# Kernel optimization log

Measured on AMD Instinct MI355X. Metric: run time of the kernel, lower is better.

## Reference

```python
import jax, jax.numpy as jnp
import numpy as np

TARGET_LEN = 288
HIDDEN = 128
INPUT_SIZE = 7
OUT_SIZE = 3  # len(quantiles)
BATCH = 1024
SEQ = 288


def _lstm_cell(x_t, h, c, Wih, Whh, b):
    # PyTorch LSTM gate order: i, f, g, o; z: (B, 4H)
    z = x_t @ Wih.T + h @ Whh.T + b
    i, f, g, o = jnp.split(z, 4, axis=-1)
    c_new = jax.nn.sigmoid(f) * c + jax.nn.sigmoid(i) * jnp.tanh(g)
    h_new = jax.nn.sigmoid(o) * jnp.tanh(c_new)
    return h_new, c_new


def setup_inputs() -> dict:
    key = jax.random.key(0)
    ks = jax.random.split(key, 11)
    s = 0.08  # ~ 1/sqrt(hidden), matches torch LSTM uniform init scale
    return {
        "x": jax.random.normal(ks[0], (BATCH, SEQ, INPUT_SIZE), jnp.float32),
        "enc_Wih": jax.random.normal(ks[1], (4 * HIDDEN, INPUT_SIZE), jnp.float32) * s,
        "enc_Whh": jax.random.normal(ks[2], (4 * HIDDEN, HIDDEN), jnp.float32) * s,
        "enc_bih": jax.random.normal(ks[3], (4 * HIDDEN,), jnp.float32) * s,
        "enc_bhh": jax.random.normal(ks[4], (4 * HIDDEN,), jnp.float32) * s,
        "dec_Wih": jax.random.normal(ks[5], (4 * HIDDEN, OUT_SIZE), jnp.float32) * s,
        "dec_Whh": jax.random.normal(ks[6], (4 * HIDDEN, HIDDEN), jnp.float32) * s,
        "dec_bih": jax.random.normal(ks[7], (4 * HIDDEN,), jnp.float32) * s,
        "dec_bhh": jax.random.normal(ks[8], (4 * HIDDEN,), jnp.float32) * s,
        "out_W": jax.random.normal(ks[9], (OUT_SIZE, HIDDEN), jnp.float32) * s,
        "out_b": jax.random.normal(ks[10], (OUT_SIZE,), jnp.float32) * s,
    }


def reference(x, enc_Wih, enc_Whh, enc_bih, enc_bhh,
              dec_Wih, dec_Whh, dec_bih, dec_bhh, out_W, out_b):
    B = x.shape[0]
    H = enc_Whh.shape[1]
    b_enc = enc_bih + enc_bhh
    b_dec = dec_bih + dec_bhh

    # ----- encoder LSTM over the input sequence -----
    def enc_step(carry, x_t):
        h, c = carry
        h, c = _lstm_cell(x_t, h, c, enc_Wih, enc_Whh, b_enc)
        return (h, c), None

    h0 = jnp.zeros((B, H), x.dtype)
    (h_enc, c_enc), _ = jax.lax.scan(enc_step, (h0, h0), jnp.swapaxes(x, 0, 1))

    # returned state, so every step restarts from (h_enc, c_enc); only the
    # previous output (quantiles) feeds back. Dropout is identity (eval). -----
    def dec_step(y_prev, _):
        h, _c = _lstm_cell(y_prev, h_enc, c_enc, dec_Wih, dec_Whh, b_dec)
        y = h @ out_W.T + out_b  # (B, OUT_SIZE)
        return y, y

    y0 = jnp.zeros((B, out_W.shape[0]), x.dtype)
    _, ys = jax.lax.scan(dec_step, y0, None, length=TARGET_LEN)  # (T, B, O)
    return jnp.swapaxes(ys, 0, 1)  # (B, TARGET_LEN, OUT_SIZE)
```

## Files before the change

### kernel.cpp

```cpp
#include <hip/hip_runtime.h>

#define SEQ 288
#define INP 7
#define HID 128
#define TLEN 288
#define OUTD 3
#define XW (SEQ * INP)

typedef _Float16 f16x8 __attribute__((ext_vector_type(8)));
typedef float f32x4 __attribute__((ext_vector_type(4)));

__device__ __forceinline__ float fast_sigmoid(float x) {
    float e = __expf(-x);
    return __builtin_amdgcn_rcpf(1.0f + e);
}
__device__ __forceinline__ float fast_tanh(float x) {
    float e = __expf(-2.0f * x);
    return 2.0f * __builtin_amdgcn_rcpf(1.0f + e) - 1.0f;
}

template<int CTRL, int RM>
__device__ __forceinline__ float dpp_add(float v) {
    int t = __builtin_amdgcn_update_dpp(0, __float_as_int(v), CTRL, RM, 0xF, true);
    return v + __int_as_float(t);
}
__device__ __forceinline__ float wave_sum(float v) {
    v = dpp_add<0xB1, 0xF>(v);
    v = dpp_add<0x4E, 0xF>(v);
    v = dpp_add<0x124, 0xF>(v);
    v = dpp_add<0x128, 0xF>(v);
    v = dpp_add<0x142, 0xA>(v);
    v = dpp_add<0x143, 0xC>(v);
    return __int_as_float(__builtin_amdgcn_readlane(__float_as_int(v), 63));
}

__device__ __forceinline__ float redist4(f32x4 s) {
    int r0 = __float_as_int(s[0]), r1 = __float_as_int(s[1]);
    int r2 = __float_as_int(s[2]), r3 = __float_as_int(s[3]);
    auto p02 = __builtin_amdgcn_permlane32_swap(r0, r2, false, false);
    auto p13 = __builtin_amdgcn_permlane32_swap(r1, r3, false, false);
#if __has_builtin(__builtin_amdgcn_permlane16_swap)
    auto q = __builtin_amdgcn_permlane16_swap(p02[0], p13[0], false, false);
    return __int_as_float(q[0]);
#else
    float n0 = __int_as_float(p02[0]);
    float n1 = __int_as_float(p13[0]);
    int lane = threadIdx.x & 63;
    float tshf = __shfl(n1, lane ^ 16);
    return (lane & 16) ? tshf : n0;
#endif
}

__global__ __launch_bounds__(512, 2)
void enc_dec_kernel(const float* __restrict__ x,
                    const float* __restrict__ eWih, const float* __restrict__ eWhh,
                    const float* __restrict__ ebih, const float* __restrict__ ebhh,
                    const float* __restrict__ dWih, const float* __restrict__ dWhh,
                    const float* __restrict__ dbih, const float* __restrict__ dbhh,
                    const float* __restrict__ oW,  const float* __restrict__ ob,
                    float* __restrict__ out)
{
    __shared__ __align__(16) _Float16 hbuf[2][4][16][40];
    __shared__ __align__(16) _Float16 xf16[SEQ + 1][4][8];
    __shared__ float zbl[4][4][HID];
    __shared__ float cl[4][HID];

    const int tid  = threadIdx.x;
    const int wave = tid >> 6;
    const int lane = tid & 63;
    const int col  = lane & 15;
    const int grp  = lane >> 4;
    const int u    = wave * 16 + col;
    const int bb   = grp;
    const int b0   = blockIdx.x * 4;

    {
        _Float16* hb = &hbuf[0][0][0][0];
        for (int i = tid; i < 2 * 4 * 16 * 40; i += 512) hb[i] = (_Float16)0.f;
        _Float16* xp = &xf16[SEQ][0][0];
        if (tid < 32) xp[tid] = (_Float16)0.f;
    }
    for (int i = tid; i < 4 * XW; i += 512) {
        int b = i / XW, r = i % XW;
        int t = r / INP, j = r % INP;
        xf16[t][b][j] = (_Float16)x[(size_t)(b0 + b) * XW + r];
    }
    for (int i = tid; i < SEQ * 4; i += 512)
        xf16[i >> 2][i & 3][7] = (_Float16)1.0f;

    f16x8 wfrag[4][5];
    #pragma unroll
    for (int gt = 0; gt < 4; ++gt) {
        const int row = gt * HID + u;
        #pragma unroll
        for (int kc = 0; kc < 4; ++kc) {
            const float* wr = eWhh + (size_t)row * HID + kc * 32 + grp * 8;
            f16x8 wf;
            #pragma unroll
            for (int e = 0; e < 8; ++e) wf[e] = (_Float16)wr[e];
            wfrag[gt][kc] = wf;
        }
        {
            f16x8 wf;
            #pragma unroll
            for (int e = 0; e < 8; ++e) {
                int j = grp * 8 + e;
                float v = 0.f;
                if (j < INP)       v = eWih[(size_t)row * INP + j];
                else if (j == 7)   v = ebih[row] + ebhh[row];
                wf[e] = (_Float16)v;
            }
            wfrag[gt][4] = wf;
        }
    }

    __syncthreads();

    float cc = 0.f;
    const f32x4 zero = (f32x4){0.f, 0.f, 0.f, 0.f};

    f32x4 accX[4];
    {
        f16x8 ax0 = *(const f16x8*)&xf16[0][col & 3][0];
        #pragma unroll
        for (int gt = 0; gt < 4; ++gt)
            accX[gt] = __builtin_amdgcn_mfma_f32_16x16x32_f16(ax0, wfrag[gt][4], zero, 0, 0, 0);
    }

    #define ENC_STEP(T, CUR, NXT)                                                     \
    {                                                                                 \
        f16x8 af0 = *(const f16x8*)&hbuf[CUR][0][col][grp * 8];                       \
        f16x8 af1 = *(const f16x8*)&hbuf[CUR][1][col][grp * 8];                       \
        f16x8 af2 = *(const f16x8*)&hbuf[CUR][2][col][grp * 8];                       \
        f16x8 af3 = *(const f16x8*)&hbuf[CUR][3][col][grp * 8];                       \
        f32x4 acc[4];                                                                 \
        _Pragma("unroll")                                                             \
        for (int gt = 0; gt < 4; ++gt) {                                              \
            acc[gt] = __builtin_amdgcn_mfma_f32_16x16x32_f16(af0, wfrag[gt][0], accX[gt], 0, 0, 0); \
            acc[gt] = __builtin_amdgcn_mfma_f32_16x16x32_f16(af1, wfrag[gt][1], acc[gt], 0, 0, 0);  \
            acc[gt] = __builtin_amdgcn_mfma_f32_16x16x32_f16(af2, wfrag[gt][2], acc[gt], 0, 0, 0);  \
            acc[gt] = __builtin_amdgcn_mfma_f32_16x16x32_f16(af3, wfrag[gt][3], acc[gt], 0, 0, 0);  \
        }                                                                             \
        f16x8 axn = *(const f16x8*)&xf16[(T) + 1][col & 3][0];                        \
        _Pragma("unroll")                                                             \
        for (int gt = 0; gt < 4; ++gt)                                                \
            accX[gt] = __builtin_amdgcn_mfma_f32_16x16x32_f16(axn, wfrag[gt][4], zero, 0, 0, 0);    \
        float zi = redist4(acc[0]);                                                   \
        float zf = redist4(acc[1]);                                                   \
        float zg = redist4(acc[2]);                                                   \
        float zo = redist4(acc[3]);                                                   \
        float si = fast_sigmoid(zi);                                                  \
        float sf = fast_sigmoid(zf);                                                  \
        float tg = fast_tanh(zg);                                                     \
        float so = fast_sigmoid(zo);                                                  \
        cc = sf * cc + si * tg;                                                       \
        float h = so * fast_tanh(cc);                                                 \
        hbuf[NXT][u >> 5][bb][u & 31] = (_Float16)h;                                  \
        __syncthreads();                                                              \
    }

    for (int t = 0; t < SEQ; t += 2) {
        ENC_STEP(t, 0, 1)
        ENC_STEP(t + 1, 1, 0)
    }
    #undef ENC_STEP

    #pragma unroll
    for (int gt = 0; gt < 4; ++gt) {
        const int row = gt * HID + u;
        #pragma unroll
        for (int kc = 0; kc < 4; ++kc) {
            const float* wr = dWhh + (size_t)row * HID + kc * 32 + grp * 8;
            f16x8 wf;
            #pragma unroll
            for (int e = 0; e < 8; ++e) wf[e] = (_Float16)wr[e];
            wfrag[gt][kc] = wf;
        }
    }
    {
        f16x8 af0 = *(const f16x8*)&hbuf[0][0][col][grp * 8];
        f16x8 af1 = *(const f16x8*)&hbuf[0][1][col][grp * 8];
        f16x8 af2 = *(const f16x8*)&hbuf[0][2][col][grp * 8];
        f16x8 af3 = *(const f16x8*)&hbuf[0][3][col][grp * 8];
        #pragma unroll
        for (int gt = 0; gt < 4; ++gt) {
            float bd = dbih[gt * HID + u] + dbhh[gt * HID + u];
            f32x4 acc = (f32x4){bd, bd, bd, bd};
            acc = __builtin_amdgcn_mfma_f32_16x16x32_f16(af0, wfrag[gt][0], acc, 0, 0, 0);
            acc = __builtin_amdgcn_mfma_f32_16x16x32_f16(af1, wfrag[gt][1], acc, 0, 0, 0);
            acc = __builtin_amdgcn_mfma_f32_16x16x32_f16(af2, wfrag[gt][2], acc, 0, 0, 0);
            acc = __builtin_amdgcn_mfma_f32_16x16x32_f16(af3, wfrag[gt][3], acc, 0, 0, 0);
            zbl[gt][bb][u] = redist4(acc);
        }
        cl[bb][u] = cc;
    }
    __syncthreads();

    if (wave >= 4) return;
    {
        const int b = wave;
        const int u0 = lane, u1 = 64 + lane;
        float zb0[4], zb1[4], wd0[4][3], wd1[4][3];
        #pragma unroll
        for (int gt = 0; gt < 4; ++gt) {
            zb0[gt] = zbl[gt][b][u0];
            zb1[gt] = zbl[gt][b][u1];
            #pragma unroll
            for (int j = 0; j < 3; ++j) {
                wd0[gt][j] = dWih[(size_t)(gt * HID + u0) * 3 + j];
                wd1[gt][j] = dWih[(size_t)(gt * HID + u1) * 3 + j];
            }
        }
        const float c0 = cl[b][u0], c1 = cl[b][u1];
        float ow0[3], ow1[3];
        #pragma unroll
        for (int j = 0; j < 3; ++j) {
            ow0[j] = oW[j * HID + u0];
            ow1[j] = oW[j * HID + u1];
        }
        const float ob0 = ob[0], ob1 = ob[1], ob2 = ob[2];

        float y0 = 0.f, y1 = 0.f, y2 = 0.f;
        float* orow = out + (size_t)(b0 + b) * (TLEN * OUTD);

        for (int t = 0; t < TLEN; ++t) {
            float z0[4], z1[4];
            #pragma unroll
            for (int gt = 0; gt < 4; ++gt) {
                z0[gt] = zb0[gt] + wd0[gt][0] * y0 + wd0[gt][1] * y1 + wd0[gt][2] * y2;
                z1[gt] = zb1[gt] + wd1[gt][0] * y0 + wd1[gt][1] * y1 + wd1[gt][2] * y2;
            }
            float si0 = fast_sigmoid(z0[0]), sf0 = fast_sigmoid(z0[1]);
            float tg0 = fast_tanh(z0[2]),    so0 = fast_sigmoid(z0[3]);
            float si1 = fast_sigmoid(z1[0]), sf1 = fast_sigmoid(z1[1]);
            float tg1 = fast_tanh(z1[2]),    so1 = fast_sigmoid(z1[3]);
            float cd0 = sf0 * c0 + si0 * tg0;
            float cd1 = sf1 * c1 + si1 * tg1;
            float hd0 = so0 * fast_tanh(cd0);
            float hd1 = so1 * fast_tanh(cd1);
            float p0 = ow0[0] * hd0 + ow1[0] * hd1;
            float p1 = ow0[1] * hd0 + ow1[1] * hd1;
            float p2 = ow0[2] * hd0 + ow1[2] * hd1;
            y0 = wave_sum(p0) + ob0;
            y1 = wave_sum(p1) + ob1;
            y2 = wave_sum(p2) + ob2;
            if (lane < 3)
                orow[t * OUTD + lane] = (lane == 0) ? y0 : (lane == 1) ? y1 : y2;
        }
    }
}

extern "C" void kernel_launch(void* const* d_in, const int* in_sizes, int n_in,
                              void* d_out, int out_size, void* d_ws, size_t ws_size,
                              hipStream_t stream) {
    (void)in_sizes; (void)n_in; (void)d_ws; (void)ws_size; (void)out_size;
    enc_dec_kernel<<<256, 512, 0, stream>>>(
        (const float*)d_in[0],
        (const float*)d_in[1], (const float*)d_in[2],
        (const float*)d_in[3], (const float*)d_in[4],
        (const float*)d_in[5], (const float*)d_in[6],
        (const float*)d_in[7], (const float*)d_in[8],
        (const float*)d_in[9], (const float*)d_in[10],
        (float*)d_out);
}
```

Measured before the change: 290.6 us.

## Split batch to two rows per block with four waves each owning thirty-two units

Each block now handles two batch rows instead of four, using 256 threads, and launches 512 blocks. Each wave computes two 16-unit tiles of gates and merges the MFMA outputs with an extra permlane swap. The aim is to spread the serial recurrence across more CUs and to use smaller per-step barriers. In exchange, half of every MFMA's batch rows carry padding, so useful matrix throughput per instruction is halved, and each wave holds twice as many weight fragments in registers.

```diff
diff --git a/kernel.cpp b/kernel.cpp
--- a/kernel.cpp
+++ b/kernel.cpp
@@ -6,6 +6,7 @@
 #define TLEN 288
 #define OUTD 3
 #define XW (SEQ * INP)
+#define BPB 2
 
 typedef _Float16 f16x8 __attribute__((ext_vector_type(8)));
 typedef float f32x4 __attribute__((ext_vector_type(4)));
@@ -51,7 +52,15 @@
 #endif
 }
 
-__global__ __launch_bounds__(512, 2)
+__device__ __forceinline__ float combine2(f32x4 a0, f32x4 a1) {
+    float z0 = redist4(a0);
+    float z1 = redist4(a1);
+    auto pr = __builtin_amdgcn_permlane32_swap(__float_as_int(z0),
+                                               __float_as_int(z1), false, false);
+    return __int_as_float(pr[0]);
+}
+
+__global__ __launch_bounds__(256, 2)
 void enc_dec_kernel(const float* __restrict__ x,
                     const float* __restrict__ eWih, const float* __restrict__ eWhh,
                     const float* __restrict__ ebih, const float* __restrict__ ebhh,
@@ -61,56 +70,59 @@
                     float* __restrict__ out)
 {
     __shared__ __align__(16) _Float16 hbuf[2][4][16][40];
-    __shared__ __align__(16) _Float16 xf16[SEQ + 1][4][8];
-    __shared__ float zbl[4][4][HID];
-    __shared__ float cl[4][HID];
+    __shared__ __align__(16) _Float16 xf16[SEQ + 1][BPB][8];
+    __shared__ float zbl[4][BPB][HID];
+    __shared__ float cl[BPB][HID];
 
     const int tid  = threadIdx.x;
     const int wave = tid >> 6;
     const int lane = tid & 63;
     const int col  = lane & 15;
     const int grp  = lane >> 4;
-    const int u    = wave * 16 + col;
-    const int bb   = grp;
-    const int b0   = blockIdx.x * 4;
+    const int bb   = (lane >> 4) & 1;
+    const int uu   = wave * 32 + (lane >> 5) * 16 + (lane & 15);
+    const int b0   = blockIdx.x * BPB;
 
     {
         _Float16* hb = &hbuf[0][0][0][0];
-        for (int i = tid; i < 2 * 4 * 16 * 40; i += 512) hb[i] = (_Float16)0.f;
+        for (int i = tid; i < 2 * 4 * 16 * 40; i += 256) hb[i] = (_Float16)0.f;
         _Float16* xp = &xf16[SEQ][0][0];
-        if (tid < 32) xp[tid] = (_Float16)0.f;
-    }
-    for (int i = tid; i < 4 * XW; i += 512) {
+        if (tid < BPB * 8) xp[tid] = (_Float16)0.f;
+    }
+    for (int i = tid; i < BPB * XW; i += 256) {
         int b = i / XW, r = i % XW;
         int t = r / INP, j = r % INP;
         xf16[t][b][j] = (_Float16)x[(size_t)(b0 + b) * XW + r];
     }
-    for (int i = tid; i < SEQ * 4; i += 512)
-        xf16[i >> 2][i & 3][7] = (_Float16)1.0f;
-
-    f16x8 wfrag[4][5];
+    for (int i = tid; i < SEQ * BPB; i += 256)
+        xf16[i / BPB][i % BPB][7] = (_Float16)1.0f;
+
+    f16x8 wfrag[4][2][5];
     #pragma unroll
     for (int gt = 0; gt < 4; ++gt) {
-        const int row = gt * HID + u;
-        #pragma unroll
-        for (int kc = 0; kc < 4; ++kc) {
-            const float* wr = eWhh + (size_t)row * HID + kc * 32 + grp * 8;
-            f16x8 wf;
-            #pragma unroll
-            for (int e = 0; e < 8; ++e) wf[e] = (_Float16)wr[e];
-            wfrag[gt][kc] = wf;
-        }
-        {
-            f16x8 wf;
-            #pragma unroll
-            for (int e = 0; e < 8; ++e) {
-                int j = grp * 8 + e;
-                float v = 0.f;
-                if (j < INP)       v = eWih[(size_t)row * INP + j];
-                else if (j == 7)   v = ebih[row] + ebhh[row];
-                wf[e] = (_Float16)v;
-            }
-            wfrag[gt][4] = wf;
+        #pragma unroll
+        for (int tl = 0; tl < 2; ++tl) {
+            const int row = gt * HID + wave * 32 + tl * 16 + col;
+            #pragma unroll
+            for (int kc = 0; kc < 4; ++kc) {
+                const float* wr = eWhh + (size_t)row * HID + kc * 32 + grp * 8;
+                f16x8 wf;
+                #pragma unroll
+                for (int e = 0; e < 8; ++e) wf[e] = (_Float16)wr[e];
+                wfrag[gt][tl][kc] = wf;
+            }
+            {
+                f16x8 wf;
+                #pragma unroll
+                for (int e = 0; e < 8; ++e) {
+                    int j = grp * 8 + e;
+                    float v = 0.f;
+                    if (j < INP)       v = eWih[(size_t)row * INP + j];
+                    else if (j == 7)   v = ebih[row] + ebhh[row];
+                    wf[e] = (_Float16)v;
+                }
+                wfrag[gt][tl][4] = wf;
+            }
         }
     }
 
@@ -119,12 +131,14 @@
     float cc = 0.f;
     const f32x4 zero = (f32x4){0.f, 0.f, 0.f, 0.f};
 
-    f32x4 accX[4];
-    {
-        f16x8 ax0 = *(const f16x8*)&xf16[0][col & 3][0];
+    f32x4 accX[4][2];
+    {
+        f16x8 ax0 = *(const f16x8*)&xf16[0][col & 1][0];
         #pragma unroll
         for (int gt = 0; gt < 4; ++gt)
-            accX[gt] = __builtin_amdgcn_mfma_f32_16x16x32_f16(ax0, wfrag[gt][4], zero, 0, 0, 0);
+            #pragma unroll
+            for (int tl = 0; tl < 2; ++tl)
+                accX[gt][tl] = __builtin_amdgcn_mfma_f32_16x16x32_f16(ax0, wfrag[gt][tl][4], zero, 0, 0, 0);
     }
 
     #define ENC_STEP(T, CUR, NXT)                                                     \
@@ -133,29 +147,34 @@
         f16x8 af1 = *(const f16x8*)&hbuf[CUR][1][col][grp * 8];                       \
         f16x8 af2 = *(const f16x8*)&hbuf[CUR][2][col][grp * 8];                       \
         f16x8 af3 = *(const f16x8*)&hbuf[CUR][3][col][grp * 8];                       \
-        f32x4 acc[4];                                                                 \
+        f16x8 axn = *(const f16x8*)&xf16[(T) + 1][col & 1][0];                        \
+        f32x4 acc[4][2];                                                              \
         _Pragma("unroll")                                                             \
         for (int gt = 0; gt < 4; ++gt) {                                              \
-            acc[gt] = __builtin_amdgcn_mfma_f32_16x16x32_f16(af0, wfrag[gt][0], accX[gt], 0, 0, 0); \
-            acc[gt] = __builtin_amdgcn_mfma_f32_16x16x32_f16(af1, wfrag[gt][1], acc[gt], 0, 0, 0);  \
-            acc[gt] = __builtin_amdgcn_mfma_f32_16x16x32_f16(af2, wfrag[gt][2], acc[gt], 0, 0, 0);  \
-            acc[gt] = __builtin_amdgcn_mfma_f32_16x16x32_f16(af3, wfrag[gt][3], acc[gt], 0, 0, 0);  \
+            _Pragma("unroll")                                                         \
+            for (int tl = 0; tl < 2; ++tl) {                                          \
+                acc[gt][tl] = __builtin_amdgcn_mfma_f32_16x16x32_f16(af0, wfrag[gt][tl][0], accX[gt][tl], 0, 0, 0); \
+                acc[gt][tl] = __builtin_amdgcn_mfma_f32_16x16x32_f16(af1, wfrag[gt][tl][1], acc[gt][tl], 0, 0, 0);  \
+                acc[gt][tl] = __builtin_amdgcn_mfma_f32_16x16x32_f16(af2, wfrag[gt][tl][2], acc[gt][tl], 0, 0, 0);  \
+                acc[gt][tl] = __builtin_amdgcn_mfma_f32_16x16x32_f16(af3, wfrag[gt][tl][3], acc[gt][tl], 0, 0, 0);  \
+            }                                                                         \
         }                                                                             \
-        f16x8 axn = *(const f16x8*)&xf16[(T) + 1][col & 3][0];                        \
         _Pragma("unroll")                                                             \
         for (int gt = 0; gt < 4; ++gt)                                                \
-            accX[gt] = __builtin_amdgcn_mfma_f32_16x16x32_f16(axn, wfrag[gt][4], zero, 0, 0, 0);    \
-        float zi = redist4(acc[0]);                                                   \
-        float zf = redist4(acc[1]);                                                   \
-        float zg = redist4(acc[2]);                                                   \
-        float zo = redist4(acc[3]);                                                   \
+            _Pragma("unroll")                                                         \
+            for (int tl = 0; tl < 2; ++tl)                                            \
+                accX[gt][tl] = __builtin_amdgcn_mfma_f32_16x16x32_f16(axn, wfrag[gt][tl][4], zero, 0, 0, 0); \
+        float zi = combine2(acc[0][0], acc[0][1]);                                    \
+        float zf = combine2(acc[1][0], acc[1][1]);                                    \
+        float zg = combine2(acc[2][0], acc[2][1]);                                    \
+        float zo = combine2(acc[3][0], acc[3][1]);                                    \
         float si = fast_sigmoid(zi);                                                  \
         float sf = fast_sigmoid(zf);                                                  \
         float tg = fast_tanh(zg);                                                     \
         float so = fast_sigmoid(zo);                                                  \
         cc = sf * cc + si * tg;                                                       \
         float h = so * fast_tanh(cc);                                                 \
-        hbuf[NXT][u >> 5][bb][u & 31] = (_Float16)h;                                  \
+        hbuf[NXT][uu >> 5][bb][uu & 31] = (_Float16)h;                                \
         __syncthreads();                                                              \
     }
 
@@ -167,14 +186,17 @@
 
     #pragma unroll
     for (int gt = 0; gt < 4; ++gt) {
-        const int row = gt * HID + u;
-        #pragma unroll
-        for (int kc = 0; kc < 4; ++kc) {
-            const float* wr = dWhh + (size_t)row * HID + kc * 32 + grp * 8;
-            f16x8 wf;
-            #pragma unroll
-            for (int e = 0; e < 8; ++e) wf[e] = (_Float16)wr[e];
-            wfrag[gt][kc] = wf;
+        #pragma unroll
+        for (int tl = 0; tl < 2; ++tl) {
+            const int row = gt * HID + wave * 32 + tl * 16 + col;
+            #pragma unroll
+            for (int kc = 0; kc < 4; ++kc) {
+                const float* wr = dWhh + (size_t)row * HID + kc * 32 + grp * 8;
+                f16x8 wf;
+                #pragma unroll
+                for (int e = 0; e < 8; ++e) wf[e] = (_Float16)wr[e];
+                wfrag[gt][tl][kc] = wf;
+            }
         }
     }
     {
@@ -182,21 +204,29 @@
         f16x8 af1 = *(const f16x8*)&hbuf[0][1][col][grp * 8];
         f16x8 af2 = *(const f16x8*)&hbuf[0][2][col][grp * 8];
         f16x8 af3 = *(const f16x8*)&hbuf[0][3][col][grp * 8];
+        f32x4 acc[4][2];
         #pragma unroll
         for (int gt = 0; gt < 4; ++gt) {
-            float bd = dbih[gt * HID + u] + dbhh[gt * HID + u];
-            f32x4 acc = (f32x4){bd, bd, bd, bd};
-            acc = __builtin_amdgcn_mfma_f32_16x16x32_f16(af0, wfrag[gt][0], acc, 0, 0, 0);
-            acc = __builtin_amdgcn_mfma_f32_16x16x32_f16(af1, wfrag[gt][1], acc, 0, 0, 0);
-            acc = __builtin_amdgcn_mfma_f32_16x16x32_f16(af2, wfrag[gt][2], acc, 0, 0, 0);
-            acc = __builtin_amdgcn_mfma_f32_16x16x32_f16(af3, wfrag[gt][3], acc, 0, 0, 0);
-            zbl[gt][bb][u] = redist4(acc);
-        }
-        cl[bb][u] = cc;
+            #pragma unroll
+            for (int tl = 0; tl < 2; ++tl) {
+                const int row = gt * HID + wave * 32 + tl * 16 + col;
+                float bd = dbih[row] + dbhh[row];
+                f32x4 a = (f32x4){bd, bd, bd, bd};
+                a = __builtin_amdgcn_mfma_f32_16x16x32_f16(af0, wfrag[gt][tl][0], a, 0, 0, 0);
+                a = __builtin_amdgcn_mfma_f32_16x16x32_f16(af1, wfrag[gt][tl][1], a, 0, 0, 0);
+                a = __builtin_amdgcn_mfma_f32_16x16x32_f16(af2, wfrag[gt][tl][2], a, 0, 0, 0);
+                a = __builtin_amdgcn_mfma_f32_16x16x32_f16(af3, wfrag[gt][tl][3], a, 0, 0, 0);
+                acc[gt][tl] = a;
+            }
+        }
+        #pragma unroll
+        for (int gt = 0; gt < 4; ++gt)
+            zbl[gt][bb][uu] = combine2(acc[gt][0], acc[gt][1]);
+        cl[bb][uu] = cc;
     }
     __syncthreads();
 
-    if (wave >= 4) return;
+    if (wave >= BPB) return;
     {
         const int b = wave;
         const int u0 = lane, u1 = 64 + lane;
@@ -254,7 +284,7 @@
                               void* d_out, int out_size, void* d_ws, size_t ws_size,
                               hipStream_t stream) {
     (void)in_sizes; (void)n_in; (void)d_ws; (void)ws_size; (void)out_size;
-    enc_dec_kernel<<<256, 512, 0, stream>>>(
+    enc_dec_kernel<<<512, 256, 0, stream>>>(
         (const float*)d_in[0],
         (const float*)d_in[1], (const float*)d_in[2],
         (const float*)d_in[3], (const float*)d_in[4],
```

After: 455.3 us. 1.57x slower.
